# Optimization experiments

Hardware: AMD Instinct MI355X
Metric: run time of the kernel (lower is better)

Reference implementation:

```python
import jax, jax.numpy as jnp
import numpy as np

H, DK, DV, DM = 8, 64, 64, 512
MAX_REL = 32
REL_VOCAB = 2 * MAX_REL + 1  # use_neg_dist=True
TREE_VOCAB = 64


def rel_pos_matrix(length):
    r = jnp.arange(length)
    dist = r[None, :] - r[:, None]                      # [L, L]
    dist = jnp.clip(dist, -MAX_REL, MAX_REL)
    return dist + MAX_REL                               # use_neg_dist -> shift


def setup_inputs() -> dict:
    key = jax.random.key(0)
    ks = jax.random.split(key, 16)
    B, L = 8, 1024
    s = 0.02
    return {
        "key": jax.random.normal(ks[0], (B, L, DM), jnp.float32),
        "value": jax.random.normal(ks[1], (B, L, DM), jnp.float32),
        "query": jax.random.normal(ks[2], (B, L, DM), jnp.float32),
        "mask": jnp.zeros((B, L, L), jnp.bool_),
        "rel_matrix": jax.random.randint(ks[3], (B, L, L), 0, TREE_VOCAB, jnp.int32),
        "rel_mask": jax.random.uniform(ks[4], (B, L, L), jnp.float32),
        "Wk": jax.random.normal(ks[5], (DM, H * DK), jnp.float32) * s,
        "bk": jnp.zeros((H * DK,), jnp.float32),
        "Wq": jax.random.normal(ks[6], (DM, H * DK), jnp.float32) * s,
        "bq": jnp.zeros((H * DK,), jnp.float32),
        "Wv": jax.random.normal(ks[7], (DM, H * DV), jnp.float32) * s,
        "bv": jnp.zeros((H * DV,), jnp.float32),
        "Wo": jax.random.normal(ks[8], (H * DV, DM), jnp.float32) * s,
        "bo": jnp.zeros((DM,), jnp.float32),
        "rel_emb_k": jax.random.normal(ks[9], (REL_VOCAB, DK), jnp.float32) * s,
        "rel_emb_v": jax.random.normal(ks[10], (REL_VOCAB, DV), jnp.float32) * s,
        "tree_emb": jax.random.normal(ks[11], (TREE_VOCAB, H), jnp.float32) * s,
    }


def reference(key, value, query, mask, rel_matrix, rel_mask,
              Wk, bk, Wq, bq, Wv, bv, Wo, bo, rel_emb_k, rel_emb_v, tree_emb):
    B, L, _ = key.shape

    def shape(x, d):  # (B, L, H*d) -> (B, H, L, d)
        return x.reshape(B, L, H, d).transpose(0, 2, 1, 3)

    k = shape(key @ Wk + bk, DK)       # [B,H,L,DK]
    v = shape(value @ Wv + bv, DV)     # [B,H,L,DV]
    q = shape(query @ Wq + bq, DK)     # [B,H,L,DK]

    rp = rel_pos_matrix(L)             # [L,L] int constant
    rel_k = rel_emb_k[rp]              # [L,L,DK]
    rel_v = rel_emb_v[rp]              # [L,L,DV]

    q = q / jnp.sqrt(jnp.asarray(DK, q.dtype))
    scores = jnp.einsum("bhqd,bhkd->bhqk", q, k)
    # relative_matmul(q, rel_k, transpose=True)
    scores = scores + jnp.einsum("bhqd,qkd->bhqk", q, rel_k)
    # tree-relative bias: embedding lookup [B,Q,K,H] -> [B,H,Q,K], masked
    tree_bias = tree_emb[rel_matrix].transpose(0, 3, 1, 2)
    scores = scores + tree_bias * rel_mask[:, None, :, :]

    scores = scores.astype(jnp.float32)
    scores = jnp.where(mask[:, None, :, :], -1e18, scores)
    attn = jax.nn.softmax(scores, axis=-1).astype(q.dtype)  # [B,H,Q,K]

    ctx = jnp.einsum("bhqk,bhkd->bhqd", attn, v)
    # relative_matmul(attn, rel_v, transpose=False)
    ctx = ctx + jnp.einsum("bhqk,qkd->bhqd", attn, rel_v)

    ctx = ctx.transpose(0, 2, 1, 3).reshape(B, L, H * DV)
    return ctx @ Wo + bo
```

## Files before the change

kernel.cpp:

```cpp
#include <hip/hip_runtime.h>
#include <stdint.h>

using f32x4  = __attribute__((ext_vector_type(4))) float;
using short8 = __attribute__((ext_vector_type(8))) short;
typedef unsigned short u16;
typedef unsigned int   u32;


static __device__ __forceinline__ u16 f2bf(float f) {
  union { float f; u32 u; } v; v.f = f;
  u32 r = v.u + 0x7fffu + ((v.u >> 16) & 1u);
  return (u16)(r >> 16);
}
static __device__ __forceinline__ float bf2f(u16 u) {
  union { u32 u; float f; } v; v.u = ((u32)u) << 16;
  return v.f;
}

#define GLDS16(g, l) __builtin_amdgcn_global_load_lds( \
    (const __attribute__((address_space(1))) u32*)(g), \
    (__attribute__((address_space(3))) u32*)(l), 16, 0, 0)

__global__ __launch_bounds__(256) void k_wt4(const float* __restrict__ W0, const float* __restrict__ W1,
                                             const float* __restrict__ W2, const float* __restrict__ W3,
                                             u16* __restrict__ T0, u16* __restrict__ T1,
                                             u16* __restrict__ T2, u16* __restrict__ T3) {
  const float* W = (blockIdx.z == 0) ? W0 : (blockIdx.z == 1) ? W1 : (blockIdx.z == 2) ? W2 : W3;
  u16* T = (blockIdx.z == 0) ? T0 : (blockIdx.z == 1) ? T1 : (blockIdx.z == 2) ? T2 : T3;
  __shared__ float t[32][33];
  int tx = threadIdx.x & 31, ty = threadIdx.x >> 5;
  int x0 = blockIdx.x * 32, y0 = blockIdx.y * 32;
  #pragma unroll
  for (int i = 0; i < 4; i++)
    t[ty + i*8][tx] = W[(y0 + ty + i*8) * 512 + (x0 + tx)];
  __syncthreads();
  #pragma unroll
  for (int i = 0; i < 4; i++)
    T[(x0 + ty + i*8) * 512 + (y0 + tx)] = f2bf(t[tx][ty + i*8]);
}

__global__ __launch_bounds__(256) void k_prep_rel(const float* __restrict__ rk,
                                                  const float* __restrict__ rv,
                                                  u16* __restrict__ relk80,
                                                  u16* __restrict__ relvT) {
  int i = blockIdx.x * 256 + threadIdx.x;
  if (i < 80*64) {
    int row = i >> 6;
    relk80[i] = (row < 65) ? f2bf(rk[i]) : (u16)0;
  }
  int j = i - 80*64;
  if (j >= 0 && j < 64*96) {
    int dv = j / 96, bk = j % 96;
    relvT[j] = (bk < 65) ? f2bf(rv[bk*64 + dv]) : (u16)0;
  }
}

__global__ __launch_bounds__(256) void k_cvt3(const float* __restrict__ a, const float* __restrict__ b,
                                              const float* __restrict__ c,
                                              u16* __restrict__ oa, u16* __restrict__ ob,
                                              u16* __restrict__ oc) {
  const float* src = (blockIdx.y == 0) ? a : (blockIdx.y == 1) ? b : c;
  u16* dst = (blockIdx.y == 0) ? oa : (blockIdx.y == 1) ? ob : oc;
  int i = blockIdx.x * 256 + threadIdx.x;
  float4 v = ((const float4*)src)[i];
  ushort4 o;
  o.x = f2bf(v.x); o.y = f2bf(v.y); o.z = f2bf(v.z); o.w = f2bf(v.w);
  ((ushort4*)dst)[i] = o;
}

__global__ __launch_bounds__(256) void k_pack(const int* __restrict__ rm,
                                              const float* __restrict__ rw,
                                              const unsigned char* __restrict__ mk,
                                              u32* __restrict__ outp) {
  int i = blockIdx.x * 256 + threadIdx.x;
  int4   r4 = ((const int4*)rm)[i];
  float4 w4 = ((const float4*)rw)[i];
  uchar4 m4 = ((const uchar4*)mk)[i];
  uint4 o;
  o.x = (u32)(r4.x & 63) | (m4.x ? 128u : 0u) | ((u32)f2bf(w4.x) << 16);
  o.y = (u32)(r4.y & 63) | (m4.y ? 128u : 0u) | ((u32)f2bf(w4.y) << 16);
  o.z = (u32)(r4.z & 63) | (m4.z ? 128u : 0u) | ((u32)f2bf(w4.z) << 16);
  o.w = (u32)(r4.w & 63) | (m4.w ? 128u : 0u) | ((u32)f2bf(w4.w) << 16);
  ((uint4*)outp)[i] = o;
}

struct GArg { const u16* A; const u16* Wt; const float* bias; void* out; int mode; float scale; };

__global__ __launch_bounds__(256) void k_gemm(GArg g0, GArg g1, GArg g2) {
  GArg ar = (blockIdx.z == 0) ? g0 : (blockIdx.z == 1) ? g1 : g2;
  __shared__ u16 As[128*32];
  __shared__ u16 Bs[64*32];
  __shared__ u16 Cs[9216];
  int tid = threadIdx.x, lane = tid & 63, wv = tid >> 6;
  int quad = lane >> 4, l15 = lane & 15;
  int n0 = blockIdx.x * 64, m0 = blockIdx.y * 128;
  int wm = (wv >> 1) * 64, wn = (wv & 1) * 32;
  f32x4 acc[4][2];
  #pragma unroll
  for (int i = 0; i < 4; i++)
    #pragma unroll
    for (int j = 0; j < 2; j++)
      acc[i][j] = (f32x4){0.f, 0.f, 0.f, 0.f};

  const u16* Abase = ar.A  + (size_t)m0 * 512;
  const u16* Bbase = ar.Wt + (size_t)n0 * 512;
  int cA0 = wv * 128, cB0 = wv * 64;

  for (int k0 = 0; k0 < 512; k0 += 32) {
    #pragma unroll
    for (int i = 0; i < 2; i++) {
      int c = cA0 + i*64 + lane;
      GLDS16(Abase + (c >> 2)*512 + k0 + (c & 3)*8, &As[(cA0 + i*64)*8]);
    }
    {
      int c = cB0 + lane;
      GLDS16(Bbase + (c >> 2)*512 + k0 + (c & 3)*8, &Bs[cB0*8]);
    }
    __syncthreads();
    short8 af[4], bf[2];
    #pragma unroll
    for (int i = 0; i < 4; i++) af[i] = *(const short8*)&As[(wm + i*16 + l15)*32 + quad*8];
    #pragma unroll
    for (int j = 0; j < 2; j++) bf[j] = *(const short8*)&Bs[(wn + j*16 + l15)*32 + quad*8];
    #pragma unroll
    for (int i = 0; i < 4; i++)
      #pragma unroll
      for (int j = 0; j < 2; j++)
        acc[i][j] = __builtin_amdgcn_mfma_f32_16x16x32_bf16(af[i], bf[j], acc[i][j], 0, 0, 0);
    __syncthreads();
  }

  if (ar.mode == 0) {
    #pragma unroll
    for (int i = 0; i < 4; i++)
      #pragma unroll
      for (int j = 0; j < 2; j++) {
        int ncol = n0 + wn + j*16 + l15;
        float bv = ar.bias[ncol];
        #pragma unroll
        for (int r = 0; r < 4; r++) {
          int m = m0 + wm + i*16 + quad*4 + r;
          ((float*)ar.out)[m*512 + ncol] = (acc[i][j][r] + bv) * ar.scale;
        }
      }
  } else {
    #pragma unroll
    for (int i = 0; i < 4; i++)
      #pragma unroll
      for (int j = 0; j < 2; j++) {
        int nloc = wn + j*16 + l15;
        float bv = ar.bias[n0 + nloc];
        #pragma unroll
        for (int r = 0; r < 4; r++) {
          int mloc = wm + i*16 + quad*4 + r;
          float val = (acc[i][j][r] + bv) * ar.scale;
          if (ar.mode == 1) Cs[mloc*72 + nloc] = f2bf(val);
          else              Cs[nloc*136 + mloc] = f2bf(val);
        }
      }
    __syncthreads();
    int bb = m0 >> 10, hh = n0 >> 6, mbase = m0 & 1023;
    u16* outp = (u16*)ar.out;
    if (ar.mode == 1) {
      size_t base = ((size_t)(bb*8 + hh)*1024 + mbase)*64;
      #pragma unroll
      for (int p = 0; p < 4; p++) {
        int mloc = (tid >> 3) + p*32, seg = tid & 7;
        *(short8*)(outp + base + (size_t)mloc*64 + seg*8) = *(const short8*)&Cs[mloc*72 + seg*8];
      }
    } else {
      size_t base = (size_t)(bb*8 + hh)*64*1024 + mbase;
      #pragma unroll
      for (int p = 0; p < 4; p++) {
        int d = (tid >> 4) + p*16, seg = tid & 15;
        *(short8*)(outp + base + (size_t)d*1024 + seg*8) = *(const short8*)&Cs[d*136 + seg*8];
      }
    }
  }
}

__global__ __launch_bounds__(512, 4) void k_attn(
    const u16* __restrict__ qws, const u16* __restrict__ kws, const u16* __restrict__ vtws,
    const u16* __restrict__ relk80, const u16* __restrict__ relvT,
    const float* __restrict__ tree_emb, const u32* __restrict__ packed,
    u16* __restrict__ ctx) {
  __shared__ u16 Kb[2][2048];
  __shared__ u16 Vb[2][2048];
  __shared__ u16 qdotL[8*16*68];
  __shared__ u16 PB[8][16*96];
  __shared__ u16 Pl[8][16*40];

  int tid = threadIdx.x, lane = tid & 63, wv = tid >> 6;
  int quad = lane >> 4, l15 = lane & 15;
  int qb = blockIdx.x, h = blockIdx.y, b = blockIdx.z;
  int q0 = qb * 128 + wv * 16;

  float treev = tree_emb[lane * 8 + h] * 1.44269504f;

  #pragma unroll
  for (int i = 0; i < 12; i++) ((u32*)&PB[wv][0])[lane + i*64] = 0u;

  const u16* qp = qws  + (size_t)(b*8 + h)*(1024*64);
  const u16* kp = kws  + (size_t)(b*8 + h)*(1024*64);
  const u16* vp = vtws + (size_t)(b*8 + h)*(64*1024);
  const u32* pkb = packed + ((size_t)b << 20);

  int rk = (wv & 3)*8 + (lane >> 3);
  int swk = (((lane & 7)*8) ^ ((rk & 7) << 3));
  int rv = (wv & 3)*16 + (lane >> 2);
  const u16* vsrc = vp + (size_t)rv*1024 + (((lane & 3)*8) ^ ((rv & 3) << 3));

#define STAGE(kt, nb) do { \
    if (wv < 4) GLDS16(kp + (size_t)((kt)*32 + rk)*64 + swk, &Kb[nb][wv*512]); \
    else        GLDS16(vsrc + (kt)*32, &Vb[nb][(wv & 3)*512]); \
  } while (0)

  STAGE(0, 0);

  short8 aQ[2];
  #pragma unroll
  for (int kf = 0; kf < 2; kf++)
    aQ[kf] = *(const short8*)(qp + (q0 + l15)*64 + kf*32 + quad*8);

  float qd0[4], qd64[4];
  #pragma unroll
  for (int t = 0; t < 5; t++) {
    f32x4 C = (f32x4){0.f,0.f,0.f,0.f};
    #pragma unroll
    for (int kf = 0; kf < 2; kf++) {
      short8 bR = *(const short8*)(relk80 + (t*16 + l15)*64 + kf*32 + quad*8);
      C = __builtin_amdgcn_mfma_f32_16x16x32_bf16(aQ[kf], bR, C, 0, 0, 0);
    }
    if (t == 0) {
      #pragma unroll
      for (int r = 0; r < 4; r++) qd0[r] = __shfl(C[r], lane & 48, 64);
    }
    if (t == 4) {
      #pragma unroll
      for (int r = 0; r < 4; r++) qd64[r] = __shfl(C[r], lane & 48, 64);
    }
    int col = t*16 + l15;
    if (col < 65) {
      #pragma unroll
      for (int r = 0; r < 4; r++)
        qdotL[(wv*16 + quad*4 + r)*68 + col] = f2bf(C[r]);
    }
  }

  int t_lo = max(0, (q0 - 31) >> 5);
  int t_hi = min(31, (q0 + 46) >> 5);

  int sK = (l15 & 7) << 3;
  int kbo0 = l15*64 + ((quad*8) ^ sK);
  int kbo1 = l15*64 + (((4 + quad)*8) ^ sK);
  int vbo  = l15*32 + ((quad*8) ^ ((l15 & 3) << 3));

  u32 pk[8];
  #pragma unroll
  for (int e = 0; e < 8; e++)
    pk[e] = pkb[((q0 + quad*4 + (e & 3)) << 10) + (e >> 2)*16 + l15];

  f32x4 O[4];
  float rs[4], ts0[4], ts1[4];
  #pragma unroll
  for (int t = 0; t < 4; t++) O[t] = (f32x4){0.f,0.f,0.f,0.f};
  #pragma unroll
  for (int r = 0; r < 4; r++) { rs[r] = 0.f; ts0[r] = 0.f; ts1[r] = 0.f; }

  for (int jt = 0; jt < 32; ++jt) {
    int cur = jt & 1;
    int k0 = jt << 5;
    __syncthreads();
    if (jt < 31) STAGE(jt + 1, cur ^ 1);

    u32 pkc[8];
    #pragma unroll
    for (int e = 0; e < 8; e++) pkc[e] = pk[e];
    if (jt < 31) {
      int kn = (jt + 1) << 5;
      #pragma unroll
      for (int e = 0; e < 8; e++)
        pk[e] = pkb[((q0 + quad*4 + (e & 3)) << 10) + kn + (e >> 2)*16 + l15];
    }

    short8 kr00 = *(const short8*)&Kb[cur][kbo0];
    short8 kr01 = *(const short8*)&Kb[cur][kbo1];
    short8 kr10 = *(const short8*)&Kb[cur][1024 + kbo0];
    short8 kr11 = *(const short8*)&Kb[cur][1024 + kbo1];
    short8 vr[4];
    #pragma unroll
    for (int t = 0; t < 4; t++) vr[t] = *(const short8*)&Vb[cur][t*512 + vbo];

    f32x4 S0 = (f32x4){0.f,0.f,0.f,0.f}, S1 = (f32x4){0.f,0.f,0.f,0.f};
    __builtin_amdgcn_s_setprio(1);
    S0 = __builtin_amdgcn_mfma_f32_16x16x32_bf16(aQ[0], kr00, S0, 0, 0, 0);
    S0 = __builtin_amdgcn_mfma_f32_16x16x32_bf16(aQ[1], kr01, S0, 0, 0, 0);
    S1 = __builtin_amdgcn_mfma_f32_16x16x32_bf16(aQ[0], kr10, S1, 0, 0, 0);
    S1 = __builtin_amdgcn_mfma_f32_16x16x32_bf16(aQ[1], kr11, S1, 0, 0, 0);
    __builtin_amdgcn_s_setprio(0);
    f32x4 Scur[2] = { S0, S1 };

    if (jt < t_lo) {
      #pragma unroll
      for (int ct = 0; ct < 2; ct++) {
        #pragma unroll
        for (int r = 0; r < 4; r++) {
          u32 sg = pkc[ct*4 + r];
          float rw = __uint_as_float(sg & 0xffff0000u);
          float tb = __int_as_float(__builtin_amdgcn_ds_bpermute(
              (int)((sg & 63u) << 2), __float_as_int(treev)));
          float qm = (sg & 128u) ? -1e30f : qd0[r];
          float p = exp2f(__builtin_fmaf(tb, rw, Scur[ct][r] + qm));
          ts0[r] += p;
          Pl[wv][(quad*4 + r)*40 + ct*16 + l15] = f2bf(p);
        }
      }
    } else if (jt > t_hi) {
      #pragma unroll
      for (int ct = 0; ct < 2; ct++) {
        #pragma unroll
        for (int r = 0; r < 4; r++) {
          u32 sg = pkc[ct*4 + r];
          float rw = __uint_as_float(sg & 0xffff0000u);
          float tb = __int_as_float(__builtin_amdgcn_ds_bpermute(
              (int)((sg & 63u) << 2), __float_as_int(treev)));
          float qm = (sg & 128u) ? -1e30f : qd64[r];
          float p = exp2f(__builtin_fmaf(tb, rw, Scur[ct][r] + qm));
          ts1[r] += p;
          Pl[wv][(quad*4 + r)*40 + ct*16 + l15] = f2bf(p);
        }
      }
    } else {
      #pragma unroll
      for (int ct = 0; ct < 2; ct++) {
        #pragma unroll
        for (int r = 0; r < 4; r++) {
          int kloc = ct*16 + l15, qloc = quad*4 + r;
          int d = (k0 + kloc) - (q0 + qloc);
          int bucket = min(max(d + 32, 0), 64);
          u32 sg = pkc[ct*4 + r];
          float rw = __uint_as_float(sg & 0xffff0000u);
          float tb = __int_as_float(__builtin_amdgcn_ds_bpermute(
              (int)((sg & 63u) << 2), __float_as_int(treev)));
          float qd = bf2f(qdotL[(wv*16 + qloc)*68 + bucket]);
          float qm = (sg & 128u) ? -1e30f : qd;
          float p = exp2f(__builtin_fmaf(tb, rw, Scur[ct][r] + qm));
          if (d <= -32)      ts0[r] += p;
          else if (d >= 32)  ts1[r] += p;
          else             { rs[r] += p; PB[wv][qloc*96 + d + 32] = f2bf(p); }
          Pl[wv][qloc*40 + kloc] = f2bf(p);
        }
      }
    }

    {
      short8 aP = *(const short8*)&Pl[wv][l15*40 + quad*8];
      __builtin_amdgcn_s_setprio(1);
      #pragma unroll
      for (int t = 0; t < 4; t++)
        O[t] = __builtin_amdgcn_mfma_f32_16x16x32_bf16(aP, vr[t], O[t], 0, 0, 0);
      __builtin_amdgcn_s_setprio(0);
    }
  }
#undef STAGE

  #pragma unroll
  for (int m = 1; m < 16; m <<= 1) {
    #pragma unroll
    for (int r = 0; r < 4; r++) {
      rs[r]  += __shfl_xor(rs[r],  m, 64);
      ts0[r] += __shfl_xor(ts0[r], m, 64);
      ts1[r] += __shfl_xor(ts1[r], m, 64);
    }
  }
  if (l15 == 0) {
    #pragma unroll
    for (int r = 0; r < 4; r++) {
      PB[wv][(quad*4 + r)*96 + 0]  = f2bf(ts0[r]);
      PB[wv][(quad*4 + r)*96 + 64] = f2bf(ts1[r]);
    }
  }

  {
    short8 aB[3];
    #pragma unroll
    for (int s = 0; s < 3; s++)
      aB[s] = *(const short8*)&PB[wv][l15*96 + s*32 + quad*8];
    #pragma unroll
    for (int t = 0; t < 4; t++)
      #pragma unroll
      for (int s = 0; s < 3; s++) {
        short8 bRV = *(const short8*)(relvT + (t*16 + l15)*96 + s*32 + quad*8);
        O[t] = __builtin_amdgcn_mfma_f32_16x16x32_bf16(aB[s], bRV, O[t], 0, 0, 0);
      }
  }

  {
    float inv[4];
    #pragma unroll
    for (int r = 0; r < 4; r++) inv[r] = 1.0f / (rs[r] + ts0[r] + ts1[r]);
    #pragma unroll
    for (int t = 0; t < 4; t++)
      #pragma unroll
      for (int r = 0; r < 4; r++) {
        int qg = q0 + quad*4 + r;
        ctx[(b*1024 + qg)*512 + h*64 + t*16 + l15] = f2bf(O[t][r] * inv[r]);
      }
  }
}

extern "C" void kernel_launch(void* const* d_in, const int* in_sizes, int n_in,
                              void* d_out, int out_size, void* d_ws, size_t ws_size,
                              hipStream_t stream) {
  const float* key   = (const float*)d_in[0];
  const float* value = (const float*)d_in[1];
  const float* query = (const float*)d_in[2];
  const unsigned char* maskp = (const unsigned char*)d_in[3];
  const int*   relm  = (const int*)d_in[4];
  const float* relw  = (const float*)d_in[5];
  const float* Wk = (const float*)d_in[6];
  const float* bk = (const float*)d_in[7];
  const float* Wq = (const float*)d_in[8];
  const float* bq = (const float*)d_in[9];
  const float* Wv = (const float*)d_in[10];
  const float* bv = (const float*)d_in[11];
  const float* Wo = (const float*)d_in[12];
  const float* bo = (const float*)d_in[13];
  const float* rek = (const float*)d_in[14];
  const float* rev = (const float*)d_in[15];
  const float* te  = (const float*)d_in[16];
  (void)in_sizes; (void)n_in; (void)out_size;

  char* w = (char*)d_ws;
  size_t off = 0;
  auto alloc = [&](size_t bytes) -> void* {
    void* p = w + off; off += (bytes + 255) & ~(size_t)255; return p;
  };
  u16* WkT = (u16*)alloc((size_t)512*512*2);
  u16* WqT = (u16*)alloc((size_t)512*512*2);
  u16* WvT = (u16*)alloc((size_t)512*512*2);
  u16* WoT = (u16*)alloc((size_t)512*512*2);
  u16* qws = (u16*)alloc((size_t)8*8*1024*64*2);
  u16* kws = (u16*)alloc((size_t)8*8*1024*64*2);
  u16* vt  = (u16*)alloc((size_t)8*8*1024*64*2);
  char* shared32 = (char*)alloc((size_t)8*1024*1024*4);
  u16* xq = (u16*)shared32;
  u16* xk = (u16*)(shared32 + (size_t)8192*512*2);
  u16* xv = (u16*)(shared32 + (size_t)2*8192*512*2);
  u32* packed = (u32*)shared32;
  u16* ctxb = (u16*)alloc((size_t)8192*512*2);
  u16* relk80 = (u16*)alloc((size_t)80*64*2);
  u16* relvT  = (u16*)alloc((size_t)64*96*2);
  if (off > ws_size) return;

  k_wt4<<<dim3(16,16,4), 256, 0, stream>>>(Wk, Wq, Wv, Wo, WkT, WqT, WvT, WoT);
  k_prep_rel<<<44, 256, 0, stream>>>(rek, rev, relk80, relvT);
  k_cvt3<<<dim3(4096,3), 256, 0, stream>>>(query, key, value, xq, xk, xv);

  GArg aq { xq, WqT, bq, (void*)qws, 1, 0.18033688f };
  GArg ak { xk, WkT, bk, (void*)kws, 1, 1.0f };
  GArg av { xv, WvT, bv, (void*)vt,  2, 1.0f };
  k_gemm<<<dim3(8,64,3), 256, 0, stream>>>(aq, ak, av);

  k_pack<<<8192, 256, 0, stream>>>(relm, relw, maskp, packed);

  k_attn<<<dim3(8,8,8), 512, 0, stream>>>(qws, kws, vt, relk80, relvT, te, packed, ctxb);

  GArg ao { ctxb, WoT, bo, d_out, 0, 1.0f };
  k_gemm<<<dim3(8,64,1), 256, 0, stream>>>(ao, ao, ao);
}
```

Baseline: 320.1 us.

## Fuse preprocessing kernels, widen GEMM tiles to 128x128, use hardware exp2 and packed bf16 converts

Merges the four preprocessing kernels (weight transpose, rel-embedding prep, input conversion, mask/index packing) into one launch dispatched by block index. To allow this, the packed buffer no longer aliases the converted-input buffer. The projection GEMM tile grows from 128x64 to 128x128, with 4x4 MFMA accumulators per wave and a larger epilogue staging buffer. In attention, exp2f is replaced by raw v_exp_f32 and probabilities are converted in pairs with v_cvt_pk_bf16_f32. This trades fewer launches and more reuse for more registers and LDS, fewer GEMM blocks, and slightly different rounding and denormal handling.

```diff
diff --git a/kernel.cpp b/kernel.cpp
--- a/kernel.cpp
+++ b/kernel.cpp
@@ -16,116 +16,120 @@
   union { u32 u; float f; } v; v.u = ((u32)u) << 16;
   return v.f;
 }
+static __device__ __forceinline__ float fexp2(float x) {
+  float r;
+  asm("v_exp_f32 %0, %1" : "=v"(r) : "v"(x));
+  return r;
+}
+static __device__ __forceinline__ u32 cvtpk(float a, float b) {
+  u32 r;
+  asm("v_cvt_pk_bf16_f32 %0, %1, %2" : "=v"(r) : "v"(a), "v"(b));
+  return r;
+}
 
 #define GLDS16(g, l) __builtin_amdgcn_global_load_lds( \
     (const __attribute__((address_space(1))) u32*)(g), \
     (__attribute__((address_space(3))) u32*)(l), 16, 0, 0)
 
-__global__ __launch_bounds__(256) void k_wt4(const float* __restrict__ W0, const float* __restrict__ W1,
-                                             const float* __restrict__ W2, const float* __restrict__ W3,
-                                             u16* __restrict__ T0, u16* __restrict__ T1,
-                                             u16* __restrict__ T2, u16* __restrict__ T3) {
-  const float* W = (blockIdx.z == 0) ? W0 : (blockIdx.z == 1) ? W1 : (blockIdx.z == 2) ? W2 : W3;
-  u16* T = (blockIdx.z == 0) ? T0 : (blockIdx.z == 1) ? T1 : (blockIdx.z == 2) ? T2 : T3;
+__global__ __launch_bounds__(256) void k_pre(
+    const float* __restrict__ W0, const float* __restrict__ W1,
+    const float* __restrict__ W2, const float* __restrict__ W3,
+    u16* __restrict__ T0, u16* __restrict__ T1, u16* __restrict__ T2, u16* __restrict__ T3,
+    const float* __restrict__ rk, const float* __restrict__ rv,
+    u16* __restrict__ relk80, u16* __restrict__ relvT,
+    const float* __restrict__ q, const float* __restrict__ k, const float* __restrict__ v,
+    u16* __restrict__ xq, u16* __restrict__ xk, u16* __restrict__ xv,
+    const int* __restrict__ rm, const float* __restrict__ rw,
+    const unsigned char* __restrict__ mk, u32* __restrict__ outp) {
   __shared__ float t[32][33];
-  int tx = threadIdx.x & 31, ty = threadIdx.x >> 5;
-  int x0 = blockIdx.x * 32, y0 = blockIdx.y * 32;
-  #pragma unroll
-  for (int i = 0; i < 4; i++)
-    t[ty + i*8][tx] = W[(y0 + ty + i*8) * 512 + (x0 + tx)];
-  __syncthreads();
-  #pragma unroll
-  for (int i = 0; i < 4; i++)
-    T[(x0 + ty + i*8) * 512 + (y0 + tx)] = f2bf(t[tx][ty + i*8]);
-}
-
-__global__ __launch_bounds__(256) void k_prep_rel(const float* __restrict__ rk,
-                                                  const float* __restrict__ rv,
-                                                  u16* __restrict__ relk80,
-                                                  u16* __restrict__ relvT) {
-  int i = blockIdx.x * 256 + threadIdx.x;
-  if (i < 80*64) {
-    int row = i >> 6;
-    relk80[i] = (row < 65) ? f2bf(rk[i]) : (u16)0;
-  }
-  int j = i - 80*64;
-  if (j >= 0 && j < 64*96) {
-    int dv = j / 96, bk = j % 96;
-    relvT[j] = (bk < 65) ? f2bf(rv[bk*64 + dv]) : (u16)0;
-  }
-}
-
-__global__ __launch_bounds__(256) void k_cvt3(const float* __restrict__ a, const float* __restrict__ b,
-                                              const float* __restrict__ c,
-                                              u16* __restrict__ oa, u16* __restrict__ ob,
-                                              u16* __restrict__ oc) {
-  const float* src = (blockIdx.y == 0) ? a : (blockIdx.y == 1) ? b : c;
-  u16* dst = (blockIdx.y == 0) ? oa : (blockIdx.y == 1) ? ob : oc;
-  int i = blockIdx.x * 256 + threadIdx.x;
-  float4 v = ((const float4*)src)[i];
-  ushort4 o;
-  o.x = f2bf(v.x); o.y = f2bf(v.y); o.z = f2bf(v.z); o.w = f2bf(v.w);
-  ((ushort4*)dst)[i] = o;
-}
-
-__global__ __launch_bounds__(256) void k_pack(const int* __restrict__ rm,
-                                              const float* __restrict__ rw,
-                                              const unsigned char* __restrict__ mk,
-                                              u32* __restrict__ outp) {
-  int i = blockIdx.x * 256 + threadIdx.x;
-  int4   r4 = ((const int4*)rm)[i];
-  float4 w4 = ((const float4*)rw)[i];
-  uchar4 m4 = ((const uchar4*)mk)[i];
-  uint4 o;
-  o.x = (u32)(r4.x & 63) | (m4.x ? 128u : 0u) | ((u32)f2bf(w4.x) << 16);
-  o.y = (u32)(r4.y & 63) | (m4.y ? 128u : 0u) | ((u32)f2bf(w4.y) << 16);
-  o.z = (u32)(r4.z & 63) | (m4.z ? 128u : 0u) | ((u32)f2bf(w4.z) << 16);
-  o.w = (u32)(r4.w & 63) | (m4.w ? 128u : 0u) | ((u32)f2bf(w4.w) << 16);
-  ((uint4*)outp)[i] = o;
+  int bid = blockIdx.x, tid = threadIdx.x;
+  if (bid < 1024) {
+    int mat = bid >> 8, rem = bid & 255;
+    const float* W = (mat == 0) ? W0 : (mat == 1) ? W1 : (mat == 2) ? W2 : W3;
+    u16* T = (mat == 0) ? T0 : (mat == 1) ? T1 : (mat == 2) ? T2 : T3;
+    int tx = tid & 31, ty = tid >> 5;
+    int x0 = (rem & 15) * 32, y0 = (rem >> 4) * 32;
+    #pragma unroll
+    for (int i = 0; i < 4; i++)
+      t[ty + i*8][tx] = W[(y0 + ty + i*8) * 512 + (x0 + tx)];
+    __syncthreads();
+    #pragma unroll
+    for (int i = 0; i < 4; i++)
+      T[(x0 + ty + i*8) * 512 + (y0 + tx)] = f2bf(t[tx][ty + i*8]);
+  } else if (bid < 1068) {
+    int i = (bid - 1024) * 256 + tid;
+    if (i < 80*64) {
+      int row = i >> 6;
+      relk80[i] = (row < 65) ? f2bf(rk[i]) : (u16)0;
+    }
+    int j = i - 80*64;
+    if (j >= 0 && j < 64*96) {
+      int dv = j / 96, bk = j % 96;
+      relvT[j] = (bk < 65) ? f2bf(rv[bk*64 + dv]) : (u16)0;
+    }
+  } else if (bid < 13356) {
+    int r = bid - 1068;
+    int z = r >> 12;
+    const float* src = (z == 0) ? q : (z == 1) ? k : v;
+    u16* dst = (z == 0) ? xq : (z == 1) ? xk : xv;
+    int i = (r & 4095) * 256 + tid;
+    float4 f = ((const float4*)src)[i];
+    ushort4 o;
+    o.x = f2bf(f.x); o.y = f2bf(f.y); o.z = f2bf(f.z); o.w = f2bf(f.w);
+    ((ushort4*)dst)[i] = o;
+  } else {
+    int i = (bid - 13356) * 256 + tid;
+    int4   r4 = ((const int4*)rm)[i];
+    float4 w4 = ((const float4*)rw)[i];
+    uchar4 m4 = ((const uchar4*)mk)[i];
+    uint4 o;
+    o.x = (u32)(r4.x & 63) | (m4.x ? 128u : 0u) | ((u32)f2bf(w4.x) << 16);
+    o.y = (u32)(r4.y & 63) | (m4.y ? 128u : 0u) | ((u32)f2bf(w4.y) << 16);
+    o.z = (u32)(r4.z & 63) | (m4.z ? 128u : 0u) | ((u32)f2bf(w4.z) << 16);
+    o.w = (u32)(r4.w & 63) | (m4.w ? 128u : 0u) | ((u32)f2bf(w4.w) << 16);
+    ((uint4*)outp)[i] = o;
+  }
 }
 
 struct GArg { const u16* A; const u16* Wt; const float* bias; void* out; int mode; float scale; };
 
-__global__ __launch_bounds__(256) void k_gemm(GArg g0, GArg g1, GArg g2) {
+__global__ __launch_bounds__(256, 3) void k_gemm(GArg g0, GArg g1, GArg g2) {
   GArg ar = (blockIdx.z == 0) ? g0 : (blockIdx.z == 1) ? g1 : g2;
   __shared__ u16 As[128*32];
-  __shared__ u16 Bs[64*32];
-  __shared__ u16 Cs[9216];
+  __shared__ u16 Bs[128*32];
+  __shared__ u16 Cs[128*136];
   int tid = threadIdx.x, lane = tid & 63, wv = tid >> 6;
   int quad = lane >> 4, l15 = lane & 15;
-  int n0 = blockIdx.x * 64, m0 = blockIdx.y * 128;
-  int wm = (wv >> 1) * 64, wn = (wv & 1) * 32;
-  f32x4 acc[4][2];
+  int n0 = blockIdx.x * 128, m0 = blockIdx.y * 128;
+  int wm = (wv >> 1) * 64, wn = (wv & 1) * 64;
+  f32x4 acc[4][4];
   #pragma unroll
   for (int i = 0; i < 4; i++)
     #pragma unroll
-    for (int j = 0; j < 2; j++)
+    for (int j = 0; j < 4; j++)
       acc[i][j] = (f32x4){0.f, 0.f, 0.f, 0.f};
 
   const u16* Abase = ar.A  + (size_t)m0 * 512;
   const u16* Bbase = ar.Wt + (size_t)n0 * 512;
-  int cA0 = wv * 128, cB0 = wv * 64;
+  int c0 = wv * 128;
 
   for (int k0 = 0; k0 < 512; k0 += 32) {
     #pragma unroll
     for (int i = 0; i < 2; i++) {
-      int c = cA0 + i*64 + lane;
-      GLDS16(Abase + (c >> 2)*512 + k0 + (c & 3)*8, &As[(cA0 + i*64)*8]);
-    }
-    {
-      int c = cB0 + lane;
-      GLDS16(Bbase + (c >> 2)*512 + k0 + (c & 3)*8, &Bs[cB0*8]);
+      int c = c0 + i*64 + lane;
+      GLDS16(Abase + (c >> 2)*512 + k0 + (c & 3)*8, &As[(c0 + i*64)*8]);
+      GLDS16(Bbase + (c >> 2)*512 + k0 + (c & 3)*8, &Bs[(c0 + i*64)*8]);
     }
     __syncthreads();
-    short8 af[4], bf[2];
+    short8 af[4], bf[4];
     #pragma unroll
     for (int i = 0; i < 4; i++) af[i] = *(const short8*)&As[(wm + i*16 + l15)*32 + quad*8];
     #pragma unroll
-    for (int j = 0; j < 2; j++) bf[j] = *(const short8*)&Bs[(wn + j*16 + l15)*32 + quad*8];
+    for (int j = 0; j < 4; j++) bf[j] = *(const short8*)&Bs[(wn + j*16 + l15)*32 + quad*8];
     #pragma unroll
     for (int i = 0; i < 4; i++)
       #pragma unroll
-      for (int j = 0; j < 2; j++)
+      for (int j = 0; j < 4; j++)
         acc[i][j] = __builtin_amdgcn_mfma_f32_16x16x32_bf16(af[i], bf[j], acc[i][j], 0, 0, 0);
     __syncthreads();
   }
@@ -134,7 +138,7 @@
     #pragma unroll
     for (int i = 0; i < 4; i++)
       #pragma unroll
-      for (int j = 0; j < 2; j++) {
+      for (int j = 0; j < 4; j++) {
         int ncol = n0 + wn + j*16 + l15;
         float bv = ar.bias[ncol];
         #pragma unroll
@@ -147,33 +151,37 @@
     #pragma unroll
     for (int i = 0; i < 4; i++)
       #pragma unroll
-      for (int j = 0; j < 2; j++) {
+      for (int j = 0; j < 4; j++) {
         int nloc = wn + j*16 + l15;
         float bv = ar.bias[n0 + nloc];
         #pragma unroll
         for (int r = 0; r < 4; r++) {
           int mloc = wm + i*16 + quad*4 + r;
           float val = (acc[i][j][r] + bv) * ar.scale;
-          if (ar.mode == 1) Cs[mloc*72 + nloc] = f2bf(val);
+          if (ar.mode == 1) Cs[mloc*136 + nloc] = f2bf(val);
           else              Cs[nloc*136 + mloc] = f2bf(val);
         }
       }
     __syncthreads();
-    int bb = m0 >> 10, hh = n0 >> 6, mbase = m0 & 1023;
+    int bb = m0 >> 10, hh0 = n0 >> 6, mbase = m0 & 1023;
     u16* outp = (u16*)ar.out;
     if (ar.mode == 1) {
-      size_t base = ((size_t)(bb*8 + hh)*1024 + mbase)*64;
-      #pragma unroll
-      for (int p = 0; p < 4; p++) {
-        int mloc = (tid >> 3) + p*32, seg = tid & 7;
-        *(short8*)(outp + base + (size_t)mloc*64 + seg*8) = *(const short8*)&Cs[mloc*72 + seg*8];
+      #pragma unroll
+      for (int p = 0; p < 8; p++) {
+        int mloc = (tid >> 4) + p*16, seg = tid & 15;
+        int head = hh0 + (seg >> 3);
+        size_t base = ((size_t)(bb*8 + head)*1024 + mbase)*64;
+        *(short8*)(outp + base + (size_t)mloc*64 + (seg & 7)*8) =
+            *(const short8*)&Cs[mloc*136 + seg*8];
       }
     } else {
-      size_t base = (size_t)(bb*8 + hh)*64*1024 + mbase;
-      #pragma unroll
-      for (int p = 0; p < 4; p++) {
-        int d = (tid >> 4) + p*16, seg = tid & 15;
-        *(short8*)(outp + base + (size_t)d*1024 + seg*8) = *(const short8*)&Cs[d*136 + seg*8];
+      #pragma unroll
+      for (int p = 0; p < 8; p++) {
+        int nloc = (tid >> 4) + p*16, seg = tid & 15;
+        int head = hh0 + (nloc >> 6), d = nloc & 63;
+        size_t base = (size_t)(bb*8 + head)*64*1024 + mbase;
+        *(short8*)(outp + base + (size_t)d*1024 + seg*8) =
+            *(const short8*)&Cs[nloc*136 + seg*8];
       }
     }
   }
@@ -303,6 +311,7 @@
     if (jt < t_lo) {
       #pragma unroll
       for (int ct = 0; ct < 2; ct++) {
+        float pv[4];
         #pragma unroll
         for (int r = 0; r < 4; r++) {
           u32 sg = pkc[ct*4 + r];
@@ -310,14 +319,19 @@
           float tb = __int_as_float(__builtin_amdgcn_ds_bpermute(
               (int)((sg & 63u) << 2), __float_as_int(treev)));
           float qm = (sg & 128u) ? -1e30f : qd0[r];
-          float p = exp2f(__builtin_fmaf(tb, rw, Scur[ct][r] + qm));
+          float p = fexp2(__builtin_fmaf(tb, rw, Scur[ct][r] + qm));
           ts0[r] += p;
-          Pl[wv][(quad*4 + r)*40 + ct*16 + l15] = f2bf(p);
+          pv[r] = p;
         }
+        u32 c01 = cvtpk(pv[0], pv[1]), c23 = cvtpk(pv[2], pv[3]);
+        u16* pl = &Pl[wv][(quad*4)*40 + ct*16 + l15];
+        pl[0]   = (u16)c01; pl[40]  = (u16)(c01 >> 16);
+        pl[80]  = (u16)c23; pl[120] = (u16)(c23 >> 16);
       }
     } else if (jt > t_hi) {
       #pragma unroll
       for (int ct = 0; ct < 2; ct++) {
+        float pv[4];
         #pragma unroll
         for (int r = 0; r < 4; r++) {
           u32 sg = pkc[ct*4 + r];
@@ -325,14 +339,19 @@
           float tb = __int_as_float(__builtin_amdgcn_ds_bpermute(
               (int)((sg & 63u) << 2), __float_as_int(treev)));
           float qm = (sg & 128u) ? -1e30f : qd64[r];
-          float p = exp2f(__builtin_fmaf(tb, rw, Scur[ct][r] + qm));
+          float p = fexp2(__builtin_fmaf(tb, rw, Scur[ct][r] + qm));
           ts1[r] += p;
-          Pl[wv][(quad*4 + r)*40 + ct*16 + l15] = f2bf(p);
+          pv[r] = p;
         }
+        u32 c01 = cvtpk(pv[0], pv[1]), c23 = cvtpk(pv[2], pv[3]);
+        u16* pl = &Pl[wv][(quad*4)*40 + ct*16 + l15];
+        pl[0]   = (u16)c01; pl[40]  = (u16)(c01 >> 16);
+        pl[80]  = (u16)c23; pl[120] = (u16)(c23 >> 16);
       }
     } else {
       #pragma unroll
       for (int ct = 0; ct < 2; ct++) {
+        float pv[4];
         #pragma unroll
         for (int r = 0; r < 4; r++) {
           int kloc = ct*16 + l15, qloc = quad*4 + r;
@@ -344,12 +363,16 @@
               (int)((sg & 63u) << 2), __float_as_int(treev)));
           float qd = bf2f(qdotL[(wv*16 + qloc)*68 + bucket]);
           float qm = (sg & 128u) ? -1e30f : qd;
-          float p = exp2f(__builtin_fmaf(tb, rw, Scur[ct][r] + qm));
+          float p = fexp2(__builtin_fmaf(tb, rw, Scur[ct][r] + qm));
           if (d <= -32)      ts0[r] += p;
           else if (d >= 32)  ts1[r] += p;
           else             { rs[r] += p; PB[wv][qloc*96 + d + 32] = f2bf(p); }
-          Pl[wv][qloc*40 + kloc] = f2bf(p);
+          pv[r] = p;
         }
+        u32 c01 = cvtpk(pv[0], pv[1]), c23 = cvtpk(pv[2], pv[3]);
+        u16* pl = &Pl[wv][(quad*4)*40 + ct*16 + l15];
+        pl[0]   = (u16)c01; pl[40]  = (u16)(c01 >> 16);
+        pl[80]  = (u16)c23; pl[120] = (u16)(c23 >> 16);
       }
     }
 
@@ -443,29 +466,27 @@
   u16* qws = (u16*)alloc((size_t)8*8*1024*64*2);
   u16* kws = (u16*)alloc((size_t)8*8*1024*64*2);
   u16* vt  = (u16*)alloc((size_t)8*8*1024*64*2);
-  char* shared32 = (char*)alloc((size_t)8*1024*1024*4);
-  u16* xq = (u16*)shared32;
-  u16* xk = (u16*)(shared32 + (size_t)8192*512*2);
-  u16* xv = (u16*)(shared32 + (size_t)2*8192*512*2);
-  u32* packed = (u32*)shared32;
+  u16* xq  = (u16*)alloc((size_t)8192*512*2);
+  u16* xk  = (u16*)alloc((size_t)8192*512*2);
+  u16* xv  = (u16*)alloc((size_t)8192*512*2);
+  u32* packed = (u32*)alloc((size_t)8*1024*1024*4);
   u16* ctxb = (u16*)alloc((size_t)8192*512*2);
   u16* relk80 = (u16*)alloc((size_t)80*64*2);
   u16* relvT  = (u16*)alloc((size_t)64*96*2);
   if (off > ws_size) return;
 
-  k_wt4<<<dim3(16,16,4), 256, 0, stream>>>(Wk, Wq, Wv, Wo, WkT, WqT, WvT, WoT);
-  k_prep_rel<<<44, 256, 0, stream>>>(rek, rev, relk80, relvT);
-  k_cvt3<<<dim3(4096,3), 256, 0, stream>>>(query, key, value, xq, xk, xv);
+  k_pre<<<21548, 256, 0, stream>>>(Wk, Wq, Wv, Wo, WkT, WqT, WvT, WoT,
+                                   rek, rev, relk80, relvT,
+                                   query, key, value, xq, xk, xv,
+                                   relm, relw, maskp, packed);
 
   GArg aq { xq, WqT, bq, (void*)qws, 1, 0.18033688f };
   GArg ak { xk, WkT, bk, (void*)kws, 1, 1.0f };
   GArg av { xv, WvT, bv, (void*)vt,  2, 1.0f };
-  k_gemm<<<dim3(8,64,3), 256, 0, stream>>>(aq, ak, av);
-
-  k_pack<<<8192, 256, 0, stream>>>(relm, relw, maskp, packed);
+  k_gemm<<<dim3(4,64,3), 256, 0, stream>>>(aq, ak, av);
 
   k_attn<<<dim3(8,8,8), 512, 0, stream>>>(qws, kws, vt, relk80, relvT, te, packed, ctxb);
 
   GArg ao { ctxb, WoT, bo, d_out, 0, 1.0f };
-  k_gemm<<<dim3(8,64,1), 256, 0, stream>>>(ao, ao, ao);
-}
+  k_gemm<<<dim3(4,64,1), 256, 0, stream>>>(ao, ao, ao);
+}
```

Result: faster. 288.8 us (-9.8%).
